# Performance work log

Measured on AMD Instinct MI355X. Metric: run time of the kernel, lower is better.

The kernel has to match this reference:

```python
import jax, jax.numpy as jnp
import numpy as np

E, B = 4, 16384
STATE, ACT, HID = 29, 8, 512
N_POSE, N_LEG = 13, 16

def _leg_inputs(state, act=None):
    # gather per-leg features: for each leg i (stride-2 over 8 joints)
    # [pos_a, vel_a, pos_b, vel_b, (act_a, act_b)] -> concat legs along batch dim
    leg = state[..., -N_LEG:]
    blocks = []
    for i in range(0, 8, 2):
        feats = [leg[..., i], leg[..., 8 + i], leg[..., i + 1], leg[..., 8 + i + 1]]
        if act is not None:
            feats += [act[..., i], act[..., i + 1]]
        blocks.append(jnp.stack(feats, axis=2))
    return jnp.concatenate(blocks, axis=1)  # [E, 4B, 4 or 6]

def _mlp(x, w0, b0, w1, b1, w2, b2, mu, sigma):
    x = (x - mu) / (sigma + 1e-8)
    x = jax.nn.relu(jnp.einsum('ebi,eih->ebh', x, w0) + b0)
    x = jax.nn.relu(jnp.einsum('ebh,ehk->ebk', x, w1) + b1)
    return jnp.einsum('ebh,eho->ebo', x, w2) + b2

def _leg_format(next_legs, b):
    # vectorized form of the original nested-loop scatter in leg_predict
    e = next_legs.shape[0]
    c = next_legs.reshape(e, 4, b, 4).transpose(0, 2, 1, 3)  # [E,B,leg,comp]
    first = jnp.stack([c[..., 0], c[..., 2]], axis=-1).reshape(e, b, 8)   # pos block
    second = jnp.stack([c[..., 1], c[..., 3]], axis=-1).reshape(e, b, 8)  # vel block
    zeros = jnp.zeros((e, b, N_POSE), next_legs.dtype)
    return jnp.concatenate([zeros, first, second], axis=-1)  # [E,B,29]

def reference(state, act, wl0, bl0, wl1, bl1, wl2, bl2, wp0, bp0, wp1, bp1, wp2, bp2,
              mu_leg, sigma_leg, mu_pose, sigma_pose,
              mu_t_leg, sigma_t_leg, mu_t_pose, sigma_t_pose):
    b = state.shape[1]
    out = _mlp(_leg_inputs(state, act), wl0, bl0, wl1, bl1, wl2, bl2, mu_leg, sigma_leg)
    legs_diff = out[..., :4] * (sigma_t_leg + 1e-8) + mu_t_leg          # [E,4B,4] mean head
    legs_curr = _leg_inputs(state)                                       # [E,4B,4]
    next_state_legs = _leg_format(legs_curr + legs_diff, b)              # [E,B,29]
    legs_diff_fmt = _leg_format(legs_diff, b)[..., -N_LEG:]              # [E,B,16]
    pose_in = jnp.concatenate([state[..., :N_POSE], legs_diff_fmt], axis=-1)  # [E,B,29]
    pose = _mlp(pose_in, wp0, bp0, wp1, bp1, wp2, bp2, mu_pose, sigma_pose)[..., :N_POSE]
    pose = pose * (sigma_t_pose + 1e-8) + mu_t_pose + state[..., :N_POSE]
    next_state = jnp.concatenate([pose, next_state_legs[..., N_POSE:]], axis=-1)
    return next_state.mean(0)  # [B, 29]

def setup_inputs():
    key = jax.random.key(0)
    ks = jax.random.split(key, 10)
    s = 0.05
    return {
        'state': jax.random.normal(ks[0], (E, B, STATE), jnp.float32),
        'act': jax.random.normal(ks[1], (E, B, ACT), jnp.float32),
        'wl0': jax.random.normal(ks[2], (E, 6, HID), jnp.float32) * s,
        'bl0': jnp.zeros((E, 1, HID), jnp.float32),
        'wl1': jax.random.normal(ks[3], (E, HID, HID), jnp.float32) * s,
        'bl1': jnp.zeros((E, 1, HID), jnp.float32),
        'wl2': jax.random.normal(ks[4], (E, HID, 8), jnp.float32) * s,
        'bl2': jnp.zeros((E, 1, 8), jnp.float32),
        'wp0': jax.random.normal(ks[5], (E, STATE, HID), jnp.float32) * s,
        'bp0': jnp.zeros((E, 1, HID), jnp.float32),
        'wp1': jax.random.normal(ks[6], (E, HID, HID), jnp.float32) * s,
        'bp1': jnp.zeros((E, 1, HID), jnp.float32),
        'wp2': jax.random.normal(ks[7], (E, HID, 2 * N_POSE), jnp.float32) * s,
        'bp2': jnp.zeros((E, 1, 2 * N_POSE), jnp.float32),
        'mu_leg': jnp.zeros((1, 6), jnp.float32),
        'sigma_leg': jnp.ones((1, 6), jnp.float32),
        'mu_pose': jnp.zeros((1, STATE), jnp.float32),
        'sigma_pose': jnp.ones((1, STATE), jnp.float32),
        'mu_t_leg': jnp.zeros((1, 4), jnp.float32),
        'sigma_t_leg': jnp.ones((1, 4), jnp.float32),
        'mu_t_pose': jnp.zeros((1, N_POSE), jnp.float32),
        'sigma_t_pose': jnp.ones((1, N_POSE), jnp.float32),
    }
```

## Files before the change

kernel.cpp:

```cpp
#include <hip/hip_runtime.h>


#define E_ 4
#define B_ 16384
#define H1S 520
#define H2S 136
#define A0S 40

typedef float f32x4 __attribute__((ext_vector_type(4)));
typedef __bf16 bf16x8 __attribute__((ext_vector_type(8)));

__device__ __forceinline__ f32x4 mfma16(bf16x8 a, bf16x8 b, f32x4 c) {
  return __builtin_amdgcn_mfma_f32_16x16x32_bf16(a, b, c, 0, 0, 0);
}

__device__ __forceinline__ void fmt_map(int k, int& ib, int& j) {
  if (k < 8) { ib = k >> 1; j = (k & 1) ? 2 : 0; }
  else { int k8 = k - 8; ib = k8 >> 1; j = (k8 & 1) ? 3 : 1; }
}

__device__ __forceinline__ void pack_one(int idx, int per_e, int KT, int Kreal,
                                         int Nsrc, int Nval,
                                         const float* __restrict__ src,
                                         const float* __restrict__ sigma,
                                         __bf16* __restrict__ dst)
{
  int e = idx / per_e;
  int rem = idx - e * per_e;
  int g = rem >> 9;
  int nt = g / KT;
  int kt = g - nt * KT;
  int li = rem & 511;
  int lane = li >> 3, j = li & 7;
  int k = kt * 32 + (lane >> 4) * 8 + j;
  int n = nt * 16 + (lane & 15);
  float v = 0.f;
  if (k < Kreal && n < Nval) {
    v = src[(size_t)e * Kreal * Nsrc + (size_t)k * Nsrc + n];
    if (sigma) v *= 1.f / (sigma[k] + 1e-8f);
  }
  dst[idx] = (__bf16)v;
}

__global__ void prep_kernel(const float* __restrict__ wl0, const float* __restrict__ wl1,
                            const float* __restrict__ wl2, const float* __restrict__ wp0,
                            const float* __restrict__ wp1, const float* __restrict__ wp2,
                            const float* __restrict__ bl0, const float* __restrict__ bp0,
                            const float* __restrict__ mu_leg, const float* __restrict__ sigma_leg,
                            const float* __restrict__ mu_pose, const float* __restrict__ sigma_pose,
                            __bf16* __restrict__ WL0p, __bf16* __restrict__ WL1p,
                            __bf16* __restrict__ WL2p, __bf16* __restrict__ WP0p,
                            __bf16* __restrict__ WP1p, __bf16* __restrict__ WP2p,
                            float* __restrict__ bl0f, float* __restrict__ bp0f)
{
  const int S0 = 65536, S1 = 1048576, S2 = 32768;
  const int total = 2 * (S0 + S1 + S2) + 4096;
  for (int idx0 = blockIdx.x * blockDim.x + threadIdx.x; idx0 < total;
       idx0 += gridDim.x * blockDim.x) {
    int x = idx0;
    if (x < S0)              { pack_one(x, 16384, 1, 6, 512, 512, wl0, sigma_leg, WL0p); }
    else if ((x -= S0) < S1) { pack_one(x, 262144, 16, 512, 512, 512, wl1, nullptr, WL1p); }
    else if ((x -= S1) < S2) { pack_one(x, 8192, 16, 512, 8, 8, wl2, nullptr, WL2p); }
    else if ((x -= S2) < S0) { pack_one(x, 16384, 1, 29, 512, 512, wp0, sigma_pose, WP0p); }
    else if ((x -= S0) < S1) { pack_one(x, 262144, 16, 512, 512, 512, wp1, nullptr, WP1p); }
    else if ((x -= S1) < S2) { pack_one(x, 8192, 16, 512, 26, 16, wp2, nullptr, WP2p); }
    else {
      x -= S2;
      if (x < 2048) {
        int e = x >> 9, n = x & 511;
        float s = bl0[e * 512 + n];
        #pragma unroll
        for (int k = 0; k < 6; ++k)
          s -= mu_leg[k] / (sigma_leg[k] + 1e-8f) * wl0[(e * 6 + k) * 512 + n];
        bl0f[e * 512 + n] = s;
      } else {
        x -= 2048;
        int e = x >> 9, n = x & 511;
        float s = bp0[e * 512 + n];
        for (int k = 0; k < 29; ++k)
          s -= mu_pose[k] / (sigma_pose[k] + 1e-8f) * wp0[(e * 29 + k) * 512 + n];
        bp0f[e * 512 + n] = s;
      }
    }
  }
}

__global__ __launch_bounds__(512) void fused_kernel(
    const float* __restrict__ state, const float* __restrict__ act,
    const float* __restrict__ bl1, const float* __restrict__ bl2,
    const float* __restrict__ bp1, const float* __restrict__ bp2,
    const float* __restrict__ mu_t_leg, const float* __restrict__ sigma_t_leg,
    const float* __restrict__ mu_t_pose, const float* __restrict__ sigma_t_pose,
    const __bf16* __restrict__ WL0p, const __bf16* __restrict__ WL1p,
    const __bf16* __restrict__ WL2p, const __bf16* __restrict__ WP0p,
    const __bf16* __restrict__ WP1p, const __bf16* __restrict__ WP2p,
    const float* __restrict__ bl0f, const float* __restrict__ bp0f,
    float* __restrict__ out)
{
  __shared__ alignas(16) __bf16 h1[128 * H1S];
  __shared__ alignas(16) __bf16 h2c[64 * H2S];
  __shared__ float ldiff[64][16];
  __shared__ float legacc[64][16];
  __bf16* a0s = h2c;

  const int tid = threadIdx.x;
  const int wv = tid >> 6;
  const int lane = tid & 63;
  const int quad = lane >> 4;
  const int l16 = lane & 15;
  const int b0 = blockIdx.x * 64;

  for (int i = tid; i < 64 * 16; i += 512) ((float*)legacc)[i] = 0.f;
  f32x4 posacc = {0.f, 0.f, 0.f, 0.f};
  __syncthreads();

  for (int e = 0; e < E_; ++e) {
    const float* se = state + (size_t)e * B_ * 29;
    const float* ae = act + (size_t)e * B_ * 8;

    for (int half = 0; half < 2; ++half) {
      __syncthreads();
      for (int i = tid; i < 128 * 32; i += 512) {
        int r = i >> 5, c = i & 31;
        float v = 0.f;
        if (c < 6) {
          int ib = r >> 5;
          int b = b0 + half * 32 + (r & 31);
          const float* sp = se + (size_t)b * 29;
          if (c == 0) v = sp[13 + 2 * ib];
          else if (c == 1) v = sp[21 + 2 * ib];
          else if (c == 2) v = sp[14 + 2 * ib];
          else if (c == 3) v = sp[22 + 2 * ib];
          else if (c == 4) v = ae[(size_t)b * 8 + 2 * ib];
          else v = ae[(size_t)b * 8 + 2 * ib + 1];
        }
        a0s[r * A0S + c] = (__bf16)v;
      }
      __syncthreads();

      {
        const __bf16* W0 = WL0p + (size_t)e * 16384;
        const float* b0v = bl0f + e * 512;
        bf16x8 bfr[4]; float bs[4];
        #pragma unroll
        for (int i = 0; i < 4; ++i) {
          int ct = wv * 4 + i;
          bfr[i] = *(const bf16x8*)(W0 + ((size_t)ct * 64 + lane) * 8);
          bs[i] = b0v[ct * 16 + l16];
        }
        for (int rt = 0; rt < 8; ++rt) {
          bf16x8 afr = *(const bf16x8*)&a0s[(rt * 16 + l16) * A0S + quad * 8];
          #pragma unroll
          for (int i = 0; i < 4; ++i) {
            f32x4 acc = {bs[i], bs[i], bs[i], bs[i]};
            acc = mfma16(afr, bfr[i], acc);
            int col = (wv * 4 + i) * 16 + l16;
            #pragma unroll
            for (int r = 0; r < 4; ++r)
              h1[(rt * 16 + quad * 4 + r) * H1S + col] = (__bf16)fmaxf(acc[r], 0.f);
          }
        }
      }
      __syncthreads();

      const __bf16* W1 = WL1p + (size_t)e * 262144;
      const __bf16* W2 = WL2p + (size_t)e * 8192;
      const float* b1v = bl1 + e * 512;
      const int rg = wv >> 2, cg = wv & 3;
      float bv2 = (l16 < 8) ? bl2[e * 8 + l16] : 0.f;
      f32x4 oacc = {bv2, bv2, bv2, bv2};

      for (int cc = 0; cc < 4; ++cc) {
        f32x4 acc[4][2];
        #pragma unroll
        for (int ct = 0; ct < 2; ++ct) {
          float bias = b1v[cc * 128 + cg * 32 + ct * 16 + l16];
          #pragma unroll
          for (int i = 0; i < 4; ++i) acc[i][ct] = (f32x4){bias, bias, bias, bias};
        }
        const __bf16* Wc = W1 + (size_t)(cc * 8 + cg * 2) * 8192;
        #pragma unroll 4
        for (int kt = 0; kt < 16; ++kt) {
          bf16x8 afr[4];
          #pragma unroll
          for (int i = 0; i < 4; ++i)
            afr[i] = *(const bf16x8*)&h1[(rg * 64 + i * 16 + l16) * H1S + kt * 32 + quad * 8];
          #pragma unroll
          for (int ct = 0; ct < 2; ++ct) {
            bf16x8 bfr = *(const bf16x8*)(Wc + (((size_t)ct * 16 + kt) * 64 + lane) * 8);
            #pragma unroll
            for (int i = 0; i < 4; ++i) acc[i][ct] = mfma16(afr[i], bfr, acc[i][ct]);
          }
        }
        #pragma unroll
        for (int hh = 0; hh < 2; ++hh) {
          __syncthreads();
          if (rg == hh) {
            #pragma unroll
            for (int i = 0; i < 4; ++i)
              #pragma unroll
              for (int ct = 0; ct < 2; ++ct)
                #pragma unroll
                for (int r = 0; r < 4; ++r)
                  h2c[(i * 16 + quad * 4 + r) * H2S + cg * 32 + ct * 16 + l16] =
                      (__bf16)fmaxf(acc[i][ct][r], 0.f);
          }
          __syncthreads();
          if ((wv >> 2) == hh) {
            #pragma unroll
            for (int k2 = 0; k2 < 4; ++k2) {
              bf16x8 afr2 = *(const bf16x8*)&h2c[((wv & 3) * 16 + l16) * H2S + k2 * 32 + quad * 8];
              bf16x8 bfr2 = *(const bf16x8*)(W2 + ((size_t)(cc * 4 + k2) * 64 + lane) * 8);
              oacc = mfma16(afr2, bfr2, oacc);
            }
          }
        }
      }
      if (l16 < 4) {
        float sc = sigma_t_leg[l16] + 1e-8f;
        float mv = mu_t_leg[l16];
        #pragma unroll
        for (int r = 0; r < 4; ++r) {
          int L = wv * 16 + quad * 4 + r;
          ldiff[half * 32 + (L & 31)][(L >> 5) * 4 + l16] = oacc[r] * sc + mv;
        }
      }
    }

    __syncthreads();
    for (int i = tid; i < 64 * 32; i += 512) {
      int t = i >> 5, c = i & 31;
      float v = 0.f;
      if (c < 13) v = se[(size_t)(b0 + t) * 29 + c];
      else if (c < 29) { int ib, j; fmt_map(c - 13, ib, j); v = ldiff[t][ib * 4 + j]; }
      a0s[t * A0S + c] = (__bf16)v;
    }
    for (int i = tid; i < 64 * 16; i += 512) {
      int t = i >> 4, k = i & 15;
      int ib, j; fmt_map(k, ib, j);
      legacc[t][k] += se[(size_t)(b0 + t) * 29 + 13 + k] + ldiff[t][ib * 4 + j];
    }
    __syncthreads();

    {
      const __bf16* W0 = WP0p + (size_t)e * 16384;
      const float* b0v = bp0f + e * 512;
      bf16x8 bfr[4]; float bs[4];
      #pragma unroll
      for (int i = 0; i < 4; ++i) {
        int ct = wv * 4 + i;
        bfr[i] = *(const bf16x8*)(W0 + ((size_t)ct * 64 + lane) * 8);
        bs[i] = b0v[ct * 16 + l16];
      }
      for (int rt = 0; rt < 4; ++rt) {
        bf16x8 afr = *(const bf16x8*)&a0s[(rt * 16 + l16) * A0S + quad * 8];
        #pragma unroll
        for (int i = 0; i < 4; ++i) {
          f32x4 acc = {bs[i], bs[i], bs[i], bs[i]};
          acc = mfma16(afr, bfr[i], acc);
          int col = (wv * 4 + i) * 16 + l16;
          #pragma unroll
          for (int r = 0; r < 4; ++r)
            h1[(rt * 16 + quad * 4 + r) * H1S + col] = (__bf16)fmaxf(acc[r], 0.f);
        }
      }
    }
    __syncthreads();

    {
      const __bf16* W1 = WP1p + (size_t)e * 262144;
      const __bf16* W2 = WP2p + (size_t)e * 8192;
      const float* b1v = bp1 + e * 512;
      float bvp = bp2[e * 26 + l16];
      f32x4 po = {bvp, bvp, bvp, bvp};

      for (int cc2 = 0; cc2 < 2; ++cc2) {
        f32x4 acc[4][2];
        #pragma unroll
        for (int ct = 0; ct < 2; ++ct) {
          float bias = b1v[cc2 * 256 + wv * 32 + ct * 16 + l16];
          #pragma unroll
          for (int i = 0; i < 4; ++i) acc[i][ct] = (f32x4){bias, bias, bias, bias};
        }
        const __bf16* Wc = W1 + (size_t)(cc2 * 16 + wv * 2) * 8192;
        #pragma unroll 4
        for (int kt = 0; kt < 16; ++kt) {
          bf16x8 afr[4];
          #pragma unroll
          for (int i = 0; i < 4; ++i)
            afr[i] = *(const bf16x8*)&h1[(i * 16 + l16) * H1S + kt * 32 + quad * 8];
          #pragma unroll
          for (int ct = 0; ct < 2; ++ct) {
            bf16x8 bfr = *(const bf16x8*)(Wc + (((size_t)ct * 16 + kt) * 64 + lane) * 8);
            #pragma unroll
            for (int i = 0; i < 4; ++i) acc[i][ct] = mfma16(afr[i], bfr, acc[i][ct]);
          }
        }
        #pragma unroll
        for (int hh = 0; hh < 2; ++hh) {
          __syncthreads();
          if ((wv >> 2) == hh) {
            int cgl = wv & 3;
            #pragma unroll
            for (int i = 0; i < 4; ++i)
              #pragma unroll
              for (int ct = 0; ct < 2; ++ct)
                #pragma unroll
                for (int r = 0; r < 4; ++r)
                  h2c[(i * 16 + quad * 4 + r) * H2S + cgl * 32 + ct * 16 + l16] =
                      (__bf16)fmaxf(acc[i][ct][r], 0.f);
          }
          __syncthreads();
          if (wv < 4) {
            #pragma unroll
            for (int k2 = 0; k2 < 4; ++k2) {
              bf16x8 afr2 = *(const bf16x8*)&h2c[(wv * 16 + l16) * H2S + k2 * 32 + quad * 8];
              bf16x8 bfr2 = *(const bf16x8*)(W2 + ((size_t)(cc2 * 8 + hh * 4 + k2) * 64 + lane) * 8);
              po = mfma16(afr2, bfr2, po);
            }
          }
        }
      }
      if (wv < 4 && l16 < 13) {
        float sc = sigma_t_pose[l16] + 1e-8f;
        float mv = mu_t_pose[l16];
        #pragma unroll
        for (int r = 0; r < 4; ++r) {
          int row = wv * 16 + quad * 4 + r;
          posacc[r] += po[r] * sc + mv + se[(size_t)(b0 + row) * 29 + l16];
        }
      }
    }
  }

  if (wv < 4 && l16 < 13) {
    #pragma unroll
    for (int r = 0; r < 4; ++r) {
      int row = wv * 16 + quad * 4 + r;
      out[(size_t)(b0 + row) * 29 + l16] = 0.25f * posacc[r];
    }
  }
  for (int i = tid; i < 64 * 16; i += 512) {
    int t = i >> 4, k = i & 15;
    out[(size_t)(b0 + t) * 29 + 13 + k] = 0.25f * legacc[t][k];
  }
}

extern "C" void kernel_launch(void* const* d_in, const int* in_sizes, int n_in,
                              void* d_out, int out_size, void* d_ws, size_t ws_size,
                              hipStream_t stream) {
  const float* state = (const float*)d_in[0];
  const float* act = (const float*)d_in[1];
  const float* wl0 = (const float*)d_in[2];
  const float* bl0 = (const float*)d_in[3];
  const float* wl1 = (const float*)d_in[4];
  const float* bl1 = (const float*)d_in[5];
  const float* wl2 = (const float*)d_in[6];
  const float* bl2 = (const float*)d_in[7];
  const float* wp0 = (const float*)d_in[8];
  const float* bp0 = (const float*)d_in[9];
  const float* wp1 = (const float*)d_in[10];
  const float* bp1 = (const float*)d_in[11];
  const float* wp2 = (const float*)d_in[12];
  const float* bp2 = (const float*)d_in[13];
  const float* mu_leg = (const float*)d_in[14];
  const float* sigma_leg = (const float*)d_in[15];
  const float* mu_pose = (const float*)d_in[16];
  const float* sigma_pose = (const float*)d_in[17];
  const float* mu_t_leg = (const float*)d_in[18];
  const float* sigma_t_leg = (const float*)d_in[19];
  const float* mu_t_pose = (const float*)d_in[20];
  const float* sigma_t_pose = (const float*)d_in[21];
  float* out = (float*)d_out;

  char* ws = (char*)d_ws;
  __bf16* WL0p = (__bf16*)(ws);
  __bf16* WL1p = (__bf16*)(ws + 131072);
  __bf16* WL2p = (__bf16*)(ws + 2228224);
  __bf16* WP0p = (__bf16*)(ws + 2293760);
  __bf16* WP1p = (__bf16*)(ws + 2424832);
  __bf16* WP2p = (__bf16*)(ws + 4521984);
  float* bl0f = (float*)(ws + 4587520);
  float* bp0f = (float*)(ws + 4595712);

  prep_kernel<<<512, 256, 0, stream>>>(wl0, wl1, wl2, wp0, wp1, wp2, bl0, bp0,
                                       mu_leg, sigma_leg, mu_pose, sigma_pose,
                                       WL0p, WL1p, WL2p, WP0p, WP1p, WP2p,
                                       bl0f, bp0f);
  fused_kernel<<<256, 512, 0, stream>>>(state, act, bl1, bl2, bp1, bp2,
                                        mu_t_leg, sigma_t_leg, mu_t_pose, sigma_t_pose,
                                        WL0p, WL1p, WL2p, WP0p, WP1p, WP2p,
                                        bl0f, bp0f, out);
}
```

Baseline: 370.1 us.

## Transpose MFMA operand roles, fuse leg output layer into FP32 epilogue

Switches the MFMA operand roles so weights are the A operand and activations the B operand, which lets layer outputs be written to LDS as packed 4-element bf16 vectors and biases loaded as f32x4. The leg MLP's final 512x8 layer is no longer an MFMA pass through shared memory. Each wave instead multiplies its ReLU'd hidden tile by fp32 wl2 rows in registers, then reduces with cross-lane shuffles and a small LDS partial-sum buffer. This removes the per-chunk h2c staging and its extra barriers. The prep kernel is rewritten to read source weights in row-major order for coalesced reads with scattered writes, the leg accumulator moves from shared memory into registers, and the pose layer-2 loop is re-tiled into four chunks.

```diff
diff --git a/kernel.cpp b/kernel.cpp
--- a/kernel.cpp
+++ b/kernel.cpp
@@ -9,6 +9,7 @@
 
 typedef float f32x4 __attribute__((ext_vector_type(4)));
 typedef __bf16 bf16x8 __attribute__((ext_vector_type(8)));
+typedef __bf16 bf16x4 __attribute__((ext_vector_type(4)));
 
 __device__ __forceinline__ f32x4 mfma16(bf16x8 a, bf16x8 b, f32x4 c) {
   return __builtin_amdgcn_mfma_f32_16x16x32_bf16(a, b, c, 0, 0, 0);
@@ -19,53 +20,50 @@
   else { int k8 = k - 8; ib = k8 >> 1; j = (k8 & 1) ? 3 : 1; }
 }
 
-__device__ __forceinline__ void pack_one(int idx, int per_e, int KT, int Kreal,
-                                         int Nsrc, int Nval,
-                                         const float* __restrict__ src,
-                                         const float* __restrict__ sigma,
-                                         __bf16* __restrict__ dst)
-{
-  int e = idx / per_e;
-  int rem = idx - e * per_e;
-  int g = rem >> 9;
-  int nt = g / KT;
-  int kt = g - nt * KT;
-  int li = rem & 511;
-  int lane = li >> 3, j = li & 7;
-  int k = kt * 32 + (lane >> 4) * 8 + j;
-  int n = nt * 16 + (lane & 15);
-  float v = 0.f;
-  if (k < Kreal && n < Nval) {
-    v = src[(size_t)e * Kreal * Nsrc + (size_t)k * Nsrc + n];
-    if (sigma) v *= 1.f / (sigma[k] + 1e-8f);
-  }
-  dst[idx] = (__bf16)v;
+__device__ __forceinline__ int pidx(int KT, int k, int n) {
+  return (((n >> 4) * KT + (k >> 5)) * 64 + ((k >> 3) & 3) * 16 + (n & 15)) * 8 + (k & 7);
 }
 
 __global__ void prep_kernel(const float* __restrict__ wl0, const float* __restrict__ wl1,
-                            const float* __restrict__ wl2, const float* __restrict__ wp0,
-                            const float* __restrict__ wp1, const float* __restrict__ wp2,
+                            const float* __restrict__ wp0, const float* __restrict__ wp1,
+                            const float* __restrict__ wp2,
                             const float* __restrict__ bl0, const float* __restrict__ bp0,
                             const float* __restrict__ mu_leg, const float* __restrict__ sigma_leg,
                             const float* __restrict__ mu_pose, const float* __restrict__ sigma_pose,
                             __bf16* __restrict__ WL0p, __bf16* __restrict__ WL1p,
-                            __bf16* __restrict__ WL2p, __bf16* __restrict__ WP0p,
-                            __bf16* __restrict__ WP1p, __bf16* __restrict__ WP2p,
+                            __bf16* __restrict__ WP0p, __bf16* __restrict__ WP1p,
+                            __bf16* __restrict__ WP2p,
                             float* __restrict__ bl0f, float* __restrict__ bp0f)
 {
-  const int S0 = 65536, S1 = 1048576, S2 = 32768;
-  const int total = 2 * (S0 + S1 + S2) + 4096;
+  const int total = 12288 + 53248 + 1048576 + 59392 + 6144 + 1048576 + 32768 + 4096;
   for (int idx0 = blockIdx.x * blockDim.x + threadIdx.x; idx0 < total;
        idx0 += gridDim.x * blockDim.x) {
     int x = idx0;
-    if (x < S0)              { pack_one(x, 16384, 1, 6, 512, 512, wl0, sigma_leg, WL0p); }
-    else if ((x -= S0) < S1) { pack_one(x, 262144, 16, 512, 512, 512, wl1, nullptr, WL1p); }
-    else if ((x -= S1) < S2) { pack_one(x, 8192, 16, 512, 8, 8, wl2, nullptr, WL2p); }
-    else if ((x -= S2) < S0) { pack_one(x, 16384, 1, 29, 512, 512, wp0, sigma_pose, WP0p); }
-    else if ((x -= S0) < S1) { pack_one(x, 262144, 16, 512, 512, 512, wp1, nullptr, WP1p); }
-    else if ((x -= S1) < S2) { pack_one(x, 8192, 16, 512, 26, 16, wp2, nullptr, WP2p); }
-    else {
-      x -= S2;
+    if (x < 12288) {
+      int e = x / 3072, r = x - e * 3072, k = r >> 9, n = r & 511;
+      WL0p[e * 16384 + pidx(1, k, n)] =
+          (__bf16)(wl0[(e * 6 + k) * 512 + n] / (sigma_leg[k] + 1e-8f));
+    } else if ((x -= 12288) < 53248) {
+      int e = x / 13312, r = x - e * 13312, k = 6 + (r >> 9), n = r & 511;
+      WL0p[e * 16384 + pidx(1, k, n)] = (__bf16)0.f;
+    } else if ((x -= 53248) < 1048576) {
+      int e = x >> 18, r = x & 262143, k = r >> 9, n = r & 511;
+      WL1p[(size_t)e * 262144 + pidx(16, k, n)] = (__bf16)wl1[((size_t)(e * 512 + k)) * 512 + n];
+    } else if ((x -= 1048576) < 59392) {
+      int e = x / 14848, r = x - e * 14848, k = r >> 9, n = r & 511;
+      WP0p[e * 16384 + pidx(1, k, n)] =
+          (__bf16)(wp0[(e * 29 + k) * 512 + n] / (sigma_pose[k] + 1e-8f));
+    } else if ((x -= 59392) < 6144) {
+      int e = x / 1536, r = x - e * 1536, k = 29 + (r >> 9), n = r & 511;
+      WP0p[e * 16384 + pidx(1, k, n)] = (__bf16)0.f;
+    } else if ((x -= 6144) < 1048576) {
+      int e = x >> 18, r = x & 262143, k = r >> 9, n = r & 511;
+      WP1p[(size_t)e * 262144 + pidx(16, k, n)] = (__bf16)wp1[((size_t)(e * 512 + k)) * 512 + n];
+    } else if ((x -= 1048576) < 32768) {
+      int e = x >> 13, r = x & 8191, k = r >> 4, n = r & 15;
+      WP2p[e * 8192 + pidx(16, k, n)] = (__bf16)wp2[(e * 512 + k) * 26 + n];
+    } else {
+      x -= 32768;
       if (x < 2048) {
         int e = x >> 9, n = x & 511;
         float s = bl0[e * 512 + n];
@@ -89,18 +87,19 @@
     const float* __restrict__ state, const float* __restrict__ act,
     const float* __restrict__ bl1, const float* __restrict__ bl2,
     const float* __restrict__ bp1, const float* __restrict__ bp2,
+    const float* __restrict__ wl2,
     const float* __restrict__ mu_t_leg, const float* __restrict__ sigma_t_leg,
     const float* __restrict__ mu_t_pose, const float* __restrict__ sigma_t_pose,
     const __bf16* __restrict__ WL0p, const __bf16* __restrict__ WL1p,
-    const __bf16* __restrict__ WL2p, const __bf16* __restrict__ WP0p,
-    const __bf16* __restrict__ WP1p, const __bf16* __restrict__ WP2p,
+    const __bf16* __restrict__ WP0p, const __bf16* __restrict__ WP1p,
+    const __bf16* __restrict__ WP2p,
     const float* __restrict__ bl0f, const float* __restrict__ bp0f,
     float* __restrict__ out)
 {
   __shared__ alignas(16) __bf16 h1[128 * H1S];
   __shared__ alignas(16) __bf16 h2c[64 * H2S];
   __shared__ float ldiff[64][16];
-  __shared__ float legacc[64][16];
+  __shared__ float legpart[128 * 16];
   __bf16* a0s = h2c;
 
   const int tid = threadIdx.x;
@@ -110,124 +109,127 @@
   const int l16 = lane & 15;
   const int b0 = blockIdx.x * 64;
 
-  for (int i = tid; i < 64 * 16; i += 512) ((float*)legacc)[i] = 0.f;
   f32x4 posacc = {0.f, 0.f, 0.f, 0.f};
-  __syncthreads();
+  float legreg[2] = {0.f, 0.f};
 
   for (int e = 0; e < E_; ++e) {
     const float* se = state + (size_t)e * B_ * 29;
     const float* ae = act + (size_t)e * B_ * 8;
 
-    for (int half = 0; half < 2; ++half) {
-      __syncthreads();
-      for (int i = tid; i < 128 * 32; i += 512) {
-        int r = i >> 5, c = i & 31;
-        float v = 0.f;
-        if (c < 6) {
-          int ib = r >> 5;
-          int b = b0 + half * 32 + (r & 31);
-          const float* sp = se + (size_t)b * 29;
-          if (c == 0) v = sp[13 + 2 * ib];
-          else if (c == 1) v = sp[21 + 2 * ib];
-          else if (c == 2) v = sp[14 + 2 * ib];
-          else if (c == 3) v = sp[22 + 2 * ib];
-          else if (c == 4) v = ae[(size_t)b * 8 + 2 * ib];
-          else v = ae[(size_t)b * 8 + 2 * ib + 1];
-        }
-        a0s[r * A0S + c] = (__bf16)v;
-      }
-      __syncthreads();
-
-      {
-        const __bf16* W0 = WL0p + (size_t)e * 16384;
-        const float* b0v = bl0f + e * 512;
-        bf16x8 bfr[4]; float bs[4];
-        #pragma unroll
-        for (int i = 0; i < 4; ++i) {
-          int ct = wv * 4 + i;
-          bfr[i] = *(const bf16x8*)(W0 + ((size_t)ct * 64 + lane) * 8);
-          bs[i] = b0v[ct * 16 + l16];
-        }
-        for (int rt = 0; rt < 8; ++rt) {
-          bf16x8 afr = *(const bf16x8*)&a0s[(rt * 16 + l16) * A0S + quad * 8];
+    {
+      const __bf16* W0 = WL0p + e * 16384;
+      const __bf16* W1 = WL1p + (size_t)e * 262144;
+      const float* b0v = bl0f + e * 512;
+      const float* b1v = bl1 + e * 512;
+      const float* w2l = wl2 + (size_t)e * 4096;
+
+      for (int half = 0; half < 2; ++half) {
+        __syncthreads();
+        for (int i = tid; i < 128 * 32; i += 512) {
+          int r = i >> 5, c = i & 31;
+          float v = 0.f;
+          if (c < 6) {
+            int ib = r >> 5;
+            int b = b0 + half * 32 + (r & 31);
+            const float* sp = se + (size_t)b * 29;
+            if (c == 0) v = sp[13 + 2 * ib];
+            else if (c == 1) v = sp[21 + 2 * ib];
+            else if (c == 2) v = sp[14 + 2 * ib];
+            else if (c == 3) v = sp[22 + 2 * ib];
+            else if (c == 4) v = ae[(size_t)b * 8 + 2 * ib];
+            else v = ae[(size_t)b * 8 + 2 * ib + 1];
+          }
+          a0s[r * A0S + c] = (__bf16)v;
+        }
+        __syncthreads();
+
+        {
+          bf16x8 wfr[4]; f32x4 bias[4];
           #pragma unroll
           for (int i = 0; i < 4; ++i) {
-            f32x4 acc = {bs[i], bs[i], bs[i], bs[i]};
-            acc = mfma16(afr, bfr[i], acc);
-            int col = (wv * 4 + i) * 16 + l16;
-            #pragma unroll
-            for (int r = 0; r < 4; ++r)
-              h1[(rt * 16 + quad * 4 + r) * H1S + col] = (__bf16)fmaxf(acc[r], 0.f);
-          }
-        }
-      }
-      __syncthreads();
-
-      const __bf16* W1 = WL1p + (size_t)e * 262144;
-      const __bf16* W2 = WL2p + (size_t)e * 8192;
-      const float* b1v = bl1 + e * 512;
-      const int rg = wv >> 2, cg = wv & 3;
-      float bv2 = (l16 < 8) ? bl2[e * 8 + l16] : 0.f;
-      f32x4 oacc = {bv2, bv2, bv2, bv2};
-
-      for (int cc = 0; cc < 4; ++cc) {
-        f32x4 acc[4][2];
-        #pragma unroll
-        for (int ct = 0; ct < 2; ++ct) {
-          float bias = b1v[cc * 128 + cg * 32 + ct * 16 + l16];
-          #pragma unroll
-          for (int i = 0; i < 4; ++i) acc[i][ct] = (f32x4){bias, bias, bias, bias};
-        }
-        const __bf16* Wc = W1 + (size_t)(cc * 8 + cg * 2) * 8192;
-        #pragma unroll 4
-        for (int kt = 0; kt < 16; ++kt) {
-          bf16x8 afr[4];
-          #pragma unroll
-          for (int i = 0; i < 4; ++i)
-            afr[i] = *(const bf16x8*)&h1[(rg * 64 + i * 16 + l16) * H1S + kt * 32 + quad * 8];
+            int nt = wv * 4 + i;
+            wfr[i] = *(const bf16x8*)(W0 + (nt * 64 + lane) * 8);
+            bias[i] = *(const f32x4*)(b0v + nt * 16 + quad * 4);
+          }
+          for (int bt = 0; bt < 8; ++bt) {
+            bf16x8 xfr = *(const bf16x8*)&a0s[(bt * 16 + l16) * A0S + quad * 8];
+            #pragma unroll
+            for (int i = 0; i < 4; ++i) {
+              f32x4 acc = mfma16(wfr[i], xfr, bias[i]);
+              bf16x4 p;
+              #pragma unroll
+              for (int r = 0; r < 4; ++r) p[r] = (__bf16)fmaxf(acc[r], 0.f);
+              *(bf16x4*)&h1[(bt * 16 + l16) * H1S + (wv * 4 + i) * 16 + quad * 4] = p;
+            }
+          }
+        }
+        __syncthreads();
+
+        const int ng = wv >> 1;
+        const int bg = wv & 1;
+        f32x4 po[4] = {{0,0,0,0},{0,0,0,0},{0,0,0,0},{0,0,0,0}};
+        for (int cc = 0; cc < 4; ++cc) {
+          f32x4 acc[4][2];
           #pragma unroll
           for (int ct = 0; ct < 2; ++ct) {
-            bf16x8 bfr = *(const bf16x8*)(Wc + (((size_t)ct * 16 + kt) * 64 + lane) * 8);
-            #pragma unroll
-            for (int i = 0; i < 4; ++i) acc[i][ct] = mfma16(afr[i], bfr, acc[i][ct]);
-          }
-        }
-        #pragma unroll
-        for (int hh = 0; hh < 2; ++hh) {
-          __syncthreads();
-          if (rg == hh) {
-            #pragma unroll
-            for (int i = 0; i < 4; ++i)
+            f32x4 bias = *(const f32x4*)(b1v + cc * 128 + (ng * 2 + ct) * 16 + quad * 4);
+            #pragma unroll
+            for (int bb = 0; bb < 4; ++bb) acc[bb][ct] = bias;
+          }
+          const int ntb = cc * 8 + ng * 2;
+          #pragma unroll 4
+          for (int kt = 0; kt < 16; ++kt) {
+            bf16x8 wf0 = *(const bf16x8*)(W1 + ((size_t)((ntb + 0) * 16 + kt) * 64 + lane) * 8);
+            bf16x8 wf1 = *(const bf16x8*)(W1 + ((size_t)((ntb + 1) * 16 + kt) * 64 + lane) * 8);
+            bf16x8 hf[4];
+            #pragma unroll
+            for (int bb = 0; bb < 4; ++bb)
+              hf[bb] = *(const bf16x8*)&h1[((bg * 4 + bb) * 16 + l16) * H1S + kt * 32 + quad * 8];
+            #pragma unroll
+            for (int bb = 0; bb < 4; ++bb) {
+              acc[bb][0] = mfma16(wf0, hf[bb], acc[bb][0]);
+              acc[bb][1] = mfma16(wf1, hf[bb], acc[bb][1]);
+            }
+          }
+          #pragma unroll
+          for (int ct = 0; ct < 2; ++ct) {
+            #pragma unroll
+            for (int r = 0; r < 4; ++r) {
+              int n = (ntb + ct) * 16 + quad * 4 + r;
+              f32x4 w2v = *(const f32x4*)(w2l + n * 8);
               #pragma unroll
-              for (int ct = 0; ct < 2; ++ct)
-                #pragma unroll
-                for (int r = 0; r < 4; ++r)
-                  h2c[(i * 16 + quad * 4 + r) * H2S + cg * 32 + ct * 16 + l16] =
-                      (__bf16)fmaxf(acc[i][ct][r], 0.f);
-          }
-          __syncthreads();
-          if ((wv >> 2) == hh) {
-            #pragma unroll
-            for (int k2 = 0; k2 < 4; ++k2) {
-              bf16x8 afr2 = *(const bf16x8*)&h2c[((wv & 3) * 16 + l16) * H2S + k2 * 32 + quad * 8];
-              bf16x8 bfr2 = *(const bf16x8*)(W2 + ((size_t)(cc * 4 + k2) * 64 + lane) * 8);
-              oacc = mfma16(afr2, bfr2, oacc);
+              for (int bb = 0; bb < 4; ++bb) {
+                float h = fmaxf(acc[bb][ct][r], 0.f);
+                po[bb] += h * w2v;
+              }
             }
           }
         }
-      }
-      if (l16 < 4) {
-        float sc = sigma_t_leg[l16] + 1e-8f;
-        float mv = mu_t_leg[l16];
-        #pragma unroll
-        for (int r = 0; r < 4; ++r) {
-          int L = wv * 16 + quad * 4 + r;
-          ldiff[half * 32 + (L & 31)][(L >> 5) * 4 + l16] = oacc[r] * sc + mv;
-        }
-      }
-    }
-
+        #pragma unroll
+        for (int bb = 0; bb < 4; ++bb) {
+          #pragma unroll
+          for (int c = 0; c < 4; ++c) {
+            po[bb][c] += __shfl_xor(po[bb][c], 16);
+            po[bb][c] += __shfl_xor(po[bb][c], 32);
+          }
+        }
+        if (quad == 0) {
+          #pragma unroll
+          for (int bb = 0; bb < 4; ++bb)
+            *(f32x4*)&legpart[((bg * 4 + bb) * 16 + l16) * 16 + ng * 4] = po[bb];
+        }
+        __syncthreads();
+        {
+          int L = tid >> 2, o = tid & 3;
+          float s = legpart[L * 16 + o] + legpart[L * 16 + 4 + o] +
+                    legpart[L * 16 + 8 + o] + legpart[L * 16 + 12 + o] + bl2[e * 8 + o];
+          s = s * (sigma_t_leg[o] + 1e-8f) + mu_t_leg[o];
+          ldiff[half * 32 + (L & 31)][(L >> 5) * 4 + o] = s;
+        }
+      }
+    }
     __syncthreads();
+
     for (int i = tid; i < 64 * 32; i += 512) {
       int t = i >> 5, c = i & 31;
       float v = 0.f;
@@ -235,33 +237,35 @@
       else if (c < 29) { int ib, j; fmt_map(c - 13, ib, j); v = ldiff[t][ib * 4 + j]; }
       a0s[t * A0S + c] = (__bf16)v;
     }
-    for (int i = tid; i < 64 * 16; i += 512) {
-      int t = i >> 4, k = i & 15;
-      int ib, j; fmt_map(k, ib, j);
-      legacc[t][k] += se[(size_t)(b0 + t) * 29 + 13 + k] + ldiff[t][ib * 4 + j];
+    {
+      #pragma unroll
+      for (int jj = 0; jj < 2; ++jj) {
+        int idx = tid * 2 + jj, t = idx >> 4, k = idx & 15;
+        int ib, j; fmt_map(k, ib, j);
+        legreg[jj] += se[(size_t)(b0 + t) * 29 + 13 + k] + ldiff[t][ib * 4 + j];
+      }
     }
     __syncthreads();
 
     {
-      const __bf16* W0 = WP0p + (size_t)e * 16384;
+      const __bf16* W0 = WP0p + e * 16384;
       const float* b0v = bp0f + e * 512;
-      bf16x8 bfr[4]; float bs[4];
+      bf16x8 wfr[4]; f32x4 bias[4];
       #pragma unroll
       for (int i = 0; i < 4; ++i) {
-        int ct = wv * 4 + i;
-        bfr[i] = *(const bf16x8*)(W0 + ((size_t)ct * 64 + lane) * 8);
-        bs[i] = b0v[ct * 16 + l16];
-      }
-      for (int rt = 0; rt < 4; ++rt) {
-        bf16x8 afr = *(const bf16x8*)&a0s[(rt * 16 + l16) * A0S + quad * 8];
+        int nt = wv * 4 + i;
+        wfr[i] = *(const bf16x8*)(W0 + (nt * 64 + lane) * 8);
+        bias[i] = *(const f32x4*)(b0v + nt * 16 + quad * 4);
+      }
+      for (int bt = 0; bt < 4; ++bt) {
+        bf16x8 xfr = *(const bf16x8*)&a0s[(bt * 16 + l16) * A0S + quad * 8];
         #pragma unroll
         for (int i = 0; i < 4; ++i) {
-          f32x4 acc = {bs[i], bs[i], bs[i], bs[i]};
-          acc = mfma16(afr, bfr[i], acc);
-          int col = (wv * 4 + i) * 16 + l16;
-          #pragma unroll
-          for (int r = 0; r < 4; ++r)
-            h1[(rt * 16 + quad * 4 + r) * H1S + col] = (__bf16)fmaxf(acc[r], 0.f);
+          f32x4 acc = mfma16(wfr[i], xfr, bias[i]);
+          bf16x4 p;
+          #pragma unroll
+          for (int r = 0; r < 4; ++r) p[r] = (__bf16)fmaxf(acc[r], 0.f);
+          *(bf16x4*)&h1[(bt * 16 + l16) * H1S + (wv * 4 + i) * 16 + quad * 4] = p;
         }
       }
     }
@@ -269,80 +273,82 @@
 
     {
       const __bf16* W1 = WP1p + (size_t)e * 262144;
-      const __bf16* W2 = WP2p + (size_t)e * 8192;
+      const __bf16* W2 = WP2p + e * 8192;
       const float* b1v = bp1 + e * 512;
-      float bvp = bp2[e * 26 + l16];
-      f32x4 po = {bvp, bvp, bvp, bvp};
-
-      for (int cc2 = 0; cc2 < 2; ++cc2) {
-        f32x4 acc[4][2];
+      const int ng = wv >> 1;
+      const int bg = wv & 1;
+      f32x4 po;
+      #pragma unroll
+      for (int r = 0; r < 4; ++r) po[r] = bp2[e * 26 + quad * 4 + r];
+
+      for (int cc = 0; cc < 4; ++cc) {
+        f32x4 acc[2][2];
         #pragma unroll
         for (int ct = 0; ct < 2; ++ct) {
-          float bias = b1v[cc2 * 256 + wv * 32 + ct * 16 + l16];
-          #pragma unroll
-          for (int i = 0; i < 4; ++i) acc[i][ct] = (f32x4){bias, bias, bias, bias};
-        }
-        const __bf16* Wc = W1 + (size_t)(cc2 * 16 + wv * 2) * 8192;
+          f32x4 bias = *(const f32x4*)(b1v + cc * 128 + (ng * 2 + ct) * 16 + quad * 4);
+          #pragma unroll
+          for (int bb = 0; bb < 2; ++bb) acc[bb][ct] = bias;
+        }
+        const int ntb = cc * 8 + ng * 2;
         #pragma unroll 4
         for (int kt = 0; kt < 16; ++kt) {
-          bf16x8 afr[4];
-          #pragma unroll
-          for (int i = 0; i < 4; ++i)
-            afr[i] = *(const bf16x8*)&h1[(i * 16 + l16) * H1S + kt * 32 + quad * 8];
+          bf16x8 wf0 = *(const bf16x8*)(W1 + ((size_t)((ntb + 0) * 16 + kt) * 64 + lane) * 8);
+          bf16x8 wf1 = *(const bf16x8*)(W1 + ((size_t)((ntb + 1) * 16 + kt) * 64 + lane) * 8);
+          bf16x8 hf[2];
+          #pragma unroll
+          for (int bb = 0; bb < 2; ++bb)
+            hf[bb] = *(const bf16x8*)&h1[((bg * 2 + bb) * 16 + l16) * H1S + kt * 32 + quad * 8];
+          #pragma unroll
+          for (int bb = 0; bb < 2; ++bb) {
+            acc[bb][0] = mfma16(wf0, hf[bb], acc[bb][0]);
+            acc[bb][1] = mfma16(wf1, hf[bb], acc[bb][1]);
+          }
+        }
+        __syncthreads();
+        #pragma unroll
+        for (int bb = 0; bb < 2; ++bb) {
           #pragma unroll
           for (int ct = 0; ct < 2; ++ct) {
-            bf16x8 bfr = *(const bf16x8*)(Wc + (((size_t)ct * 16 + kt) * 64 + lane) * 8);
-            #pragma unroll
-            for (int i = 0; i < 4; ++i) acc[i][ct] = mfma16(afr[i], bfr, acc[i][ct]);
-          }
-        }
-        #pragma unroll
-        for (int hh = 0; hh < 2; ++hh) {
-          __syncthreads();
-          if ((wv >> 2) == hh) {
-            int cgl = wv & 3;
-            #pragma unroll
-            for (int i = 0; i < 4; ++i)
-              #pragma unroll
-              for (int ct = 0; ct < 2; ++ct)
-                #pragma unroll
-                for (int r = 0; r < 4; ++r)
-                  h2c[(i * 16 + quad * 4 + r) * H2S + cgl * 32 + ct * 16 + l16] =
-                      (__bf16)fmaxf(acc[i][ct][r], 0.f);
-          }
-          __syncthreads();
-          if (wv < 4) {
-            #pragma unroll
-            for (int k2 = 0; k2 < 4; ++k2) {
-              bf16x8 afr2 = *(const bf16x8*)&h2c[(wv * 16 + l16) * H2S + k2 * 32 + quad * 8];
-              bf16x8 bfr2 = *(const bf16x8*)(W2 + ((size_t)(cc2 * 8 + hh * 4 + k2) * 64 + lane) * 8);
-              po = mfma16(afr2, bfr2, po);
-            }
-          }
-        }
-      }
-      if (wv < 4 && l16 < 13) {
-        float sc = sigma_t_pose[l16] + 1e-8f;
-        float mv = mu_t_pose[l16];
+            bf16x4 p;
+            #pragma unroll
+            for (int r = 0; r < 4; ++r) p[r] = (__bf16)fmaxf(acc[bb][ct][r], 0.f);
+            *(bf16x4*)&h2c[((bg * 2 + bb) * 16 + l16) * H2S + (ng * 2 + ct) * 16 + quad * 4] = p;
+          }
+        }
+        __syncthreads();
+        if (wv < 4) {
+          #pragma unroll
+          for (int k2 = 0; k2 < 4; ++k2) {
+            bf16x8 hf2 = *(const bf16x8*)&h2c[(wv * 16 + l16) * H2S + k2 * 32 + quad * 8];
+            bf16x8 wf2 = *(const bf16x8*)(W2 + ((cc * 4 + k2) * 64 + lane) * 8);
+            po = mfma16(wf2, hf2, po);
+          }
+        }
+      }
+      if (wv < 4) {
         #pragma unroll
         for (int r = 0; r < 4; ++r) {
-          int row = wv * 16 + quad * 4 + r;
-          posacc[r] += po[r] * sc + mv + se[(size_t)(b0 + row) * 29 + l16];
+          int o = quad * 4 + r;
+          if (o < 13)
+            posacc[r] += po[r] * (sigma_t_pose[o] + 1e-8f) + mu_t_pose[o] +
+                         se[(size_t)(b0 + wv * 16 + l16) * 29 + o];
         }
       }
     }
   }
 
-  if (wv < 4 && l16 < 13) {
+  if (wv < 4) {
     #pragma unroll
     for (int r = 0; r < 4; ++r) {
-      int row = wv * 16 + quad * 4 + r;
-      out[(size_t)(b0 + row) * 29 + l16] = 0.25f * posacc[r];
+      int o = quad * 4 + r;
+      if (o < 13)
+        out[(size_t)(b0 + wv * 16 + l16) * 29 + o] = 0.25f * posacc[r];
     }
   }
-  for (int i = tid; i < 64 * 16; i += 512) {
-    int t = i >> 4, k = i & 15;
-    out[(size_t)(b0 + t) * 29 + 13 + k] = 0.25f * legacc[t][k];
+  #pragma unroll
+  for (int jj = 0; jj < 2; ++jj) {
+    int idx = tid * 2 + jj, t = idx >> 4, k = idx & 15;
+    out[(size_t)(b0 + t) * 29 + 13 + k] = 0.25f * legreg[jj];
   }
 }
 
@@ -376,19 +382,17 @@
   char* ws = (char*)d_ws;
   __bf16* WL0p = (__bf16*)(ws);
   __bf16* WL1p = (__bf16*)(ws + 131072);
-  __bf16* WL2p = (__bf16*)(ws + 2228224);
-  __bf16* WP0p = (__bf16*)(ws + 2293760);
-  __bf16* WP1p = (__bf16*)(ws + 2424832);
-  __bf16* WP2p = (__bf16*)(ws + 4521984);
-  float* bl0f = (float*)(ws + 4587520);
-  float* bp0f = (float*)(ws + 4595712);
-
-  prep_kernel<<<512, 256, 0, stream>>>(wl0, wl1, wl2, wp0, wp1, wp2, bl0, bp0,
+  __bf16* WP0p = (__bf16*)(ws + 2228224);
+  __bf16* WP1p = (__bf16*)(ws + 2359296);
+  __bf16* WP2p = (__bf16*)(ws + 4456448);
+  float* bl0f = (float*)(ws + 4521984);
+  float* bp0f = (float*)(ws + 4530176);
+
+  prep_kernel<<<512, 256, 0, stream>>>(wl0, wl1, wp0, wp1, wp2, bl0, bp0,
                                        mu_leg, sigma_leg, mu_pose, sigma_pose,
-                                       WL0p, WL1p, WL2p, WP0p, WP1p, WP2p,
-                                       bl0f, bp0f);
-  fused_kernel<<<256, 512, 0, stream>>>(state, act, bl1, bl2, bp1, bp2,
+                                       WL0p, WL1p, WP0p, WP1p, WP2p, bl0f, bp0f);
+  fused_kernel<<<256, 512, 0, stream>>>(state, act, bl1, bl2, bp1, bp2, wl2,
                                         mu_t_leg, sigma_t_leg, mu_t_pose, sigma_t_pose,
-                                        WL0p, WL1p, WL2p, WP0p, WP1p, WP2p,
+                                        WL0p, WL1p, WP0p, WP1p, WP2p,
                                         bl0f, bp0f, out);
 }
```

Measured after the change: 681.4 us. 1.84x slower.
